# Performance work log

Measured on AMD Instinct MI355X. Metric: run time of the kernel, lower is better.

The kernel has to match this reference:

```python
import jax, jax.numpy as jnp
import numpy as np

POOL_RAD = 1.0   # init kwarg pool_rad
N = 16384        # total points
B = 8            # graphs in batch
F = 128          # feature dim
BIG = 1e30

def _voxel_keys(pos, batch, rad):
    # torch_geometric.voxel_grid with start=min-rad/2, end=max+rad/2, batch as extra dim
    start = pos.min(0) - rad * 0.5
    end = pos.max(0) + rad * 0.5
    nv = jnp.floor((end - start) / rad).astype(jnp.int32) + 1  # voxels per spatial dim
    c = jnp.floor((pos - start) / rad).astype(jnp.int32)       # [N,3] voxel coords
    lin = c[:, 0] + c[:, 1] * nv[0] + c[:, 2] * nv[0] * nv[1]
    return lin + batch.astype(jnp.int32) * (nv[0] * nv[1] * nv[2])

def _consecutive(keys, n):
    # consecutive_cluster: relabel to sorted-consecutive ids; perm = last index per cluster
    _, inv = jnp.unique(keys, return_inverse=True, size=n,
                        fill_value=jnp.iinfo(jnp.int32).max)
    inv = inv.reshape(-1)
    perm = jax.ops.segment_max(jnp.arange(n, dtype=jnp.int32), inv, num_segments=n)
    counts = jax.ops.segment_sum(jnp.ones((n,), jnp.int32), inv, num_segments=n)
    return inv, jnp.clip(perm, 0, n - 1), counts

def _nearest(pos, batch, cpos, cbatch, cvalid):
    # nearest centroid within the same graph; invalid/padded centroids masked out
    d = (pos * pos).sum(1)[:, None] - 2.0 * (pos @ cpos.T) + (cpos * cpos).sum(1)[None, :]
    ok = (batch[:, None] == cbatch[None, :]) & cvalid[None, :]
    return jnp.argmin(jnp.where(ok, d, BIG), axis=1)

def _pool(pos, x, batch):
    n = pos.shape[0]
    # stage 1: voxel-grid clustering, centroid positions
    inv1, perm1, cnt1 = _consecutive(_voxel_keys(pos, batch, POOL_RAD), n)
    c1 = jnp.maximum(cnt1, 1).astype(pos.dtype)[:, None]
    cpos = jax.ops.segment_sum(pos, inv1, num_segments=n) / c1
    cbatch = batch[perm1]
    # stage 2: reassign each point to its nearest voxel centroid, relabel
    cl2 = _nearest(jax.lax.stop_gradient(pos), batch,
                   jax.lax.stop_gradient(cpos), cbatch, cnt1 > 0)
    inv2, perm2, cnt2 = _consecutive(cl2, n)
    valid2 = cnt2 > 0
    c2 = jnp.maximum(cnt2, 1).astype(pos.dtype)[:, None]
    pos_out = jax.ops.segment_sum(pos, inv2, num_segments=n) / c2   # mean pos
    x_out = jax.ops.segment_max(x, inv2, num_segments=n)            # aggr='max'
    x_out = jnp.where(valid2[:, None], x_out, 0.0)
    pos_out = jnp.where(valid2[:, None], pos_out, 0.0)
    batch_out = jnp.where(valid2, batch[perm2], -1)
    return x_out, pos_out, batch_out

def setup_inputs():
    key = jax.random.key(0)
    k1, k2 = jax.random.split(key)
    pos = jax.random.uniform(k1, (N, 3), jnp.float32) * 10.0
    x = jax.random.normal(k2, (N, F), jnp.float32)
    batch = jnp.repeat(jnp.arange(B, dtype=jnp.int32), N // B)
    return {"pos": pos, "x": x, "batch": batch}

def reference(pos, x, batch):
    return _pool(pos, x, batch)
```

## Files before the change

### kernel.cpp

```cpp
#include <hip/hip_runtime.h>

#define TPB 256
#define K1SZ 32768
#define MAXB 256

static __device__ __forceinline__ unsigned int fmap(float f) {
  unsigned int b = __float_as_uint(f);
  return (b & 0x80000000u) ? ~b : (b | 0x80000000u);
}
static __device__ __forceinline__ float funmap(unsigned int u) {
  unsigned int b = (u & 0x80000000u) ? (u & 0x7fffffffu) : ~u;
  return __uint_as_float(b);
}

static __device__ __forceinline__ int wave_incl_scan(int v, int lane) {
  #pragma unroll
  for (int off = 1; off < 64; off <<= 1) {
    int u = __shfl_up(v, off);
    if (lane >= off) v += u;
  }
  return v;
}

__global__ void k_init(double* __restrict__ sum1, double* __restrict__ sum2,
                       int* __restrict__ cnt1, int* __restrict__ cnt2,
                       int* __restrict__ perm1, int* __restrict__ perm2,
                       int* __restrict__ flags1, int* __restrict__ flags2,
                       unsigned int* __restrict__ xacc, int n, int F) {
  int t = blockIdx.x * blockDim.x + threadIdx.x;
  if (t < n * F) xacc[t] = 0u;
  if (t < 3 * n) { sum1[t] = 0.0; sum2[t] = 0.0; }
  if (t < n) { cnt1[t] = 0; cnt2[t] = 0; perm1[t] = -1; perm2[t] = -1; flags2[t] = 0; }
  if (t < K1SZ) flags1[t] = 0;
}

__global__ __launch_bounds__(1024) void k_minmax(const float* __restrict__ pos, int n,
                                                 float* __restrict__ scal) {
  int t = threadIdx.x;
  int lane = t & 63, wid = t >> 6;
  float mn[3] = {3.4e38f, 3.4e38f, 3.4e38f};
  float mx[3] = {-3.4e38f, -3.4e38f, -3.4e38f};
  const float4* p4 = (const float4*)pos;
  int np4 = n >> 2;
  for (int j = t; j < np4; j += 1024) {
    float4 a = p4[3 * j], b = p4[3 * j + 1], c = p4[3 * j + 2];
    mn[0] = fminf(mn[0], fminf(fminf(a.x, a.w), fminf(b.z, c.y)));
    mx[0] = fmaxf(mx[0], fmaxf(fmaxf(a.x, a.w), fmaxf(b.z, c.y)));
    mn[1] = fminf(mn[1], fminf(fminf(a.y, b.x), fminf(b.w, c.z)));
    mx[1] = fmaxf(mx[1], fmaxf(fmaxf(a.y, b.x), fmaxf(b.w, c.z)));
    mn[2] = fminf(mn[2], fminf(fminf(a.z, b.y), fminf(c.x, c.w)));
    mx[2] = fmaxf(mx[2], fmaxf(fmaxf(a.z, b.y), fmaxf(c.x, c.w)));
  }
  if (t == 0) {
    for (int i = np4 * 4; i < n; ++i)
      for (int d = 0; d < 3; ++d) {
        float v = pos[i * 3 + d];
        mn[d] = fminf(mn[d], v);
        mx[d] = fmaxf(mx[d], v);
      }
  }
  #pragma unroll
  for (int off = 32; off > 0; off >>= 1) {
    #pragma unroll
    for (int d = 0; d < 3; ++d) {
      mn[d] = fminf(mn[d], __shfl_xor(mn[d], off));
      mx[d] = fmaxf(mx[d], __shfl_xor(mx[d], off));
    }
  }
  __shared__ float smn[16][3], smx[16][3];
  if (lane == 0)
    for (int d = 0; d < 3; ++d) { smn[wid][d] = mn[d]; smx[wid][d] = mx[d]; }
  __syncthreads();
  if (t == 0) {
    float rmn[3], rmx[3];
    for (int d = 0; d < 3; ++d) { rmn[d] = smn[0][d]; rmx[d] = smx[0][d]; }
    for (int w = 1; w < 16; ++w)
      for (int d = 0; d < 3; ++d) {
        rmn[d] = fminf(rmn[d], smn[w][d]);
        rmx[d] = fmaxf(rmx[d], smx[w][d]);
      }
    int* isc = (int*)(scal + 3);
    int nv[3];
    for (int d = 0; d < 3; ++d) {
      float start = rmn[d] - 0.5f;
      float end   = rmx[d] + 0.5f;
      nv[d] = (int)floorf(end - start) + 1;
      scal[d] = start;
    }
    isc[0] = nv[0];
    isc[1] = nv[0] * nv[1];
    isc[2] = nv[0] * nv[1] * nv[2];
  }
}

__global__ void k_keys(const float* __restrict__ pos, const int* __restrict__ batch, int n,
                       const float* __restrict__ scal, int* __restrict__ key1,
                       int* __restrict__ flags1) {
  int i = blockIdx.x * blockDim.x + threadIdx.x;
  if (i >= n) return;
  const int* isc = (const int*)(scal + 3);
  int c0 = (int)floorf(pos[i * 3 + 0] - scal[0]);
  int c1 = (int)floorf(pos[i * 3 + 1] - scal[1]);
  int c2 = (int)floorf(pos[i * 3 + 2] - scal[2]);
  int key = c0 + c1 * isc[0] + c2 * isc[1] + batch[i] * isc[2];
  key = min(max(key, 0), K1SZ - 1);
  key1[i] = key;
  flags1[key] = 1;
}

__global__ __launch_bounds__(1024) void k_scan(const int* __restrict__ flags,
                                               int* __restrict__ rank, int L) {
  const int t = threadIdx.x;
  const int lane = t & 63;
  const int wid = t >> 6;
  __shared__ int wsum[16];
  const int4* f4 = (const int4*)flags;
  int4* r4 = (int4*)rank;
  const int n4 = L >> 2;
  int base = 0;
  for (int tile = 0; tile * 1024 < n4; ++tile) {
    int i = tile * 1024 + t;
    int4 v = (i < n4) ? f4[i] : int4{0, 0, 0, 0};
    int p0 = v.x, p1 = p0 + v.y, p2 = p1 + v.z, p3 = p2 + v.w;
    int ws = wave_incl_scan(p3, lane);
    if (lane == 63) wsum[wid] = ws;
    __syncthreads();
    int woff = 0, ttot = 0;
    #pragma unroll
    for (int w = 0; w < 16; ++w) {
      int s = wsum[w];
      if (w < wid) woff += s;
      ttot += s;
    }
    int e = base + woff + (ws - p3);
    if (i < n4) r4[i] = int4{e, e + p0, e + p1, e + p2};
    base += ttot;
    __syncthreads();
  }
  if (t == 0) rank[L] = base;
}

__global__ void k_assign1(const float* __restrict__ pos, int n,
                          const int* __restrict__ key1, const int* __restrict__ rank1,
                          int* __restrict__ inv1, int* __restrict__ cnt1,
                          int* __restrict__ perm1, double* __restrict__ sum1) {
  int i = blockIdx.x * blockDim.x + threadIdx.x;
  if (i >= n) return;
  int c = rank1[key1[i]];
  inv1[i] = c;
  atomicAdd(&cnt1[c], 1);
  atomicMax(&perm1[c], i);
  atomicAdd(&sum1[c * 3 + 0], (double)pos[i * 3 + 0]);
  atomicAdd(&sum1[c * 3 + 1], (double)pos[i * 3 + 1]);
  atomicAdd(&sum1[c * 3 + 2], (double)pos[i * 3 + 2]);
}

__global__ void k_centroid1(int n, const int* __restrict__ cnt1,
                            double* __restrict__ sum1,
                            const int* __restrict__ rank1, const float* __restrict__ scal,
                            int* __restrict__ blo, int* __restrict__ bhi) {
  int k = blockIdx.x * blockDim.x + threadIdx.x;
  if (k < MAXB) {
    int nvtot = ((const int*)(scal + 3))[2];
    long long j0l = (long long)k * nvtot;
    long long j1l = j0l + nvtot;
    int j0 = (int)(j0l > K1SZ ? K1SZ : j0l);
    int j1 = (int)(j1l > K1SZ ? K1SZ : j1l);
    int lo = rank1[j0], hi = rank1[j1] - 1;
    blo[k] = (hi >= lo) ? lo : -1;
    bhi[k] = hi;
  }
  if (k >= n) return;
  int c = cnt1[k];
  if (c <= 0) return;
  double inv = 1.0 / (double)c;
  sum1[k * 3 + 0] *= inv;
  sum1[k * 3 + 1] *= inv;
  sum1[k * 3 + 2] *= inv;
}

__global__ void k_nearest(const float* __restrict__ pos, const int* __restrict__ batch, int n,
                          const double* __restrict__ cpos, const int* __restrict__ blo,
                          const int* __restrict__ bhi, int* __restrict__ cl2,
                          int* __restrict__ flags2) {
  int w = (blockIdx.x * blockDim.x + threadIdx.x) >> 6;
  int lane = threadIdx.x & 63;
  if (w >= n) return;
  double px = pos[w * 3 + 0], py = pos[w * 3 + 1], pz = pos[w * 3 + 2];
  int b = min(max(batch[w], 0), MAXB - 1);
  int lo = blo[b], hi = bhi[b];
  double best = 1e300;
  int bk = lo >= 0 ? lo : 0;
  if (lo >= 0) {
    for (int k = lo + lane; k <= hi; k += 64) {
      double dx = px - cpos[k * 3 + 0];
      double dy = py - cpos[k * 3 + 1];
      double dz = pz - cpos[k * 3 + 2];
      double d = dx * dx + dy * dy + dz * dz;
      if (d < best) { best = d; bk = k; }
    }
  }
  for (int off = 32; off > 0; off >>= 1) {
    double od = __shfl_down(best, off);
    int ok = __shfl_down(bk, off);
    if (od < best || (od == best && ok < bk)) { best = od; bk = ok; }
  }
  if (lane == 0) {
    cl2[w] = bk;
    flags2[bk] = 1;
  }
}

__global__ void k_assign2(const float* __restrict__ pos, int n,
                          const int* __restrict__ cl2, const int* __restrict__ rank2,
                          int* __restrict__ inv2, int* __restrict__ cnt2,
                          int* __restrict__ perm2, double* __restrict__ sum2) {
  int i = blockIdx.x * blockDim.x + threadIdx.x;
  if (i >= n) return;
  int c = rank2[cl2[i]];
  inv2[i] = c;
  atomicAdd(&cnt2[c], 1);
  atomicMax(&perm2[c], i);
  atomicAdd(&sum2[c * 3 + 0], (double)pos[i * 3 + 0]);
  atomicAdd(&sum2[c * 3 + 1], (double)pos[i * 3 + 1]);
  atomicAdd(&sum2[c * 3 + 2], (double)pos[i * 3 + 2]);
}

__global__ void k_xmax(const float* __restrict__ x, int n, int F,
                       const int* __restrict__ inv2, unsigned int* __restrict__ xacc) {
  int t = blockIdx.x * blockDim.x + threadIdx.x;
  if (t >= n * F) return;
  int i = t / F;
  int f = t - i * F;
  atomicMax(&xacc[inv2[i] * F + f], fmap(x[t]));
}

__global__ void k_finalize(int n, int F, const int* __restrict__ cnt2,
                           const int* __restrict__ perm2, const int* __restrict__ batch,
                           const double* __restrict__ sum2, unsigned int* __restrict__ xacc,
                           float* __restrict__ pos_out, float* __restrict__ batch_out) {
  int t = blockIdx.x * blockDim.x + threadIdx.x;
  if (t < n * F) {
    int j = t / F;
    float out = 0.0f;
    if (cnt2[j] > 0) out = funmap(xacc[t]);
    ((float*)xacc)[t] = out;
  }
  if (t < n) {
    int c = cnt2[t];
    if (c > 0) {
      double inv = 1.0 / (double)c;
      pos_out[t * 3 + 0] = (float)(sum2[t * 3 + 0] * inv);
      pos_out[t * 3 + 1] = (float)(sum2[t * 3 + 1] * inv);
      pos_out[t * 3 + 2] = (float)(sum2[t * 3 + 2] * inv);
      batch_out[t] = (float)batch[perm2[t]];
    } else {
      pos_out[t * 3 + 0] = 0.0f;
      pos_out[t * 3 + 1] = 0.0f;
      pos_out[t * 3 + 2] = 0.0f;
      batch_out[t] = -1.0f;
    }
  }
}

extern "C" void kernel_launch(void* const* d_in, const int* in_sizes, int n_in,
                              void* d_out, int out_size, void* d_ws, size_t ws_size,
                              hipStream_t stream) {
  const float* pos   = (const float*)d_in[0];
  const float* x     = (const float*)d_in[1];
  const int*   batch = (const int*)d_in[2];
  int n = in_sizes[2];
  int F = in_sizes[1] / n;

  char* ws = (char*)d_ws;
  size_t off = 0;
  auto alloc = [&](size_t bytes, size_t align) -> void* {
    off = (off + align - 1) & ~(align - 1);
    void* p = ws + off;
    off += bytes;
    return p;
  };
  double* sum1   = (double*)alloc((size_t)n * 3 * sizeof(double), 16);
  double* sum2   = (double*)alloc((size_t)n * 3 * sizeof(double), 16);
  int* key1      = (int*)alloc((size_t)n * 4, 16);
  int* inv1      = (int*)alloc((size_t)n * 4, 16);
  int* cnt1      = (int*)alloc((size_t)n * 4, 16);
  int* perm1     = (int*)alloc((size_t)n * 4, 16);
  int* cl2       = (int*)alloc((size_t)n * 4, 16);
  int* inv2      = (int*)alloc((size_t)n * 4, 16);
  int* cnt2      = (int*)alloc((size_t)n * 4, 16);
  int* perm2     = (int*)alloc((size_t)n * 4, 16);
  int* flags1    = (int*)alloc((size_t)K1SZ * 4, 16);
  int* rank1     = (int*)alloc(((size_t)K1SZ + 4) * 4, 16);
  int* flags2    = (int*)alloc((size_t)n * 4, 16);
  int* rank2     = (int*)alloc(((size_t)n + 4) * 4, 16);
  int* blo       = (int*)alloc((size_t)MAXB * 4, 16);
  int* bhi       = (int*)alloc((size_t)MAXB * 4, 16);
  float* scal    = (float*)alloc(64, 16);

  unsigned int* xacc = (unsigned int*)d_out;
  float* pos_out     = (float*)d_out + (size_t)n * F;
  float* batch_out   = pos_out + (size_t)n * 3;

  int nb  = (n + TPB - 1) / TPB;
  int nbF = (n * F + TPB - 1) / TPB;
  int nbW = (n * 64 + TPB - 1) / TPB;

  k_init<<<nbF, TPB, 0, stream>>>(sum1, sum2, cnt1, cnt2, perm1, perm2,
                                  flags1, flags2, xacc, n, F);
  k_minmax<<<1, 1024, 0, stream>>>(pos, n, scal);
  k_keys<<<nb, TPB, 0, stream>>>(pos, batch, n, scal, key1, flags1);
  k_scan<<<1, 1024, 0, stream>>>(flags1, rank1, K1SZ);
  k_assign1<<<nb, TPB, 0, stream>>>(pos, n, key1, rank1, inv1, cnt1, perm1, sum1);
  k_centroid1<<<nb, TPB, 0, stream>>>(n, cnt1, sum1, rank1, scal, blo, bhi);
  k_nearest<<<nbW, TPB, 0, stream>>>(pos, batch, n, sum1, blo, bhi, cl2, flags2);
  k_scan<<<1, 1024, 0, stream>>>(flags2, rank2, n);
  k_assign2<<<nb, TPB, 0, stream>>>(pos, n, cl2, rank2, inv2, cnt2, perm2, sum2);
  k_xmax<<<nbF, TPB, 0, stream>>>(x, n, F, inv2, xacc);
  k_finalize<<<nbF, TPB, 0, stream>>>(n, F, cnt2, perm2, batch, sum2, xacc,
                                      pos_out, batch_out);
}
```

Measured before the change: 78.72 us.

## Fuse minmax, key, and scan stages into one block; merge assign2 into xmax

Merges the min/max reduction, voxel-key computation, stage-1 scan and per-batch range computation into a single 1024-thread kernel, which removes several launches and global round-trips. The second assignment is folded into the feature max kernel, with the f==0 thread doing the count, perm and sum atomics. Unused inv1/perm1 arrays and their atomics are dropped. The trade-off is that key computation now runs on only one block instead of a full grid, and the xmax kernel recomputes the rank lookup for every feature element.

```diff
diff --git a/kernel.cpp b/kernel.cpp
--- a/kernel.cpp
+++ b/kernel.cpp
@@ -24,20 +24,31 @@
 
 __global__ void k_init(double* __restrict__ sum1, double* __restrict__ sum2,
                        int* __restrict__ cnt1, int* __restrict__ cnt2,
-                       int* __restrict__ perm1, int* __restrict__ perm2,
-                       int* __restrict__ flags1, int* __restrict__ flags2,
-                       unsigned int* __restrict__ xacc, int n, int F) {
+                       int* __restrict__ perm2, int* __restrict__ flags1,
+                       int* __restrict__ flags2, unsigned int* __restrict__ xacc,
+                       int n, int F) {
   int t = blockIdx.x * blockDim.x + threadIdx.x;
   if (t < n * F) xacc[t] = 0u;
   if (t < 3 * n) { sum1[t] = 0.0; sum2[t] = 0.0; }
-  if (t < n) { cnt1[t] = 0; cnt2[t] = 0; perm1[t] = -1; perm2[t] = -1; flags2[t] = 0; }
+  if (t < n) { cnt1[t] = 0; cnt2[t] = 0; perm2[t] = -1; flags2[t] = 0; }
   if (t < K1SZ) flags1[t] = 0;
 }
 
-__global__ __launch_bounds__(1024) void k_minmax(const float* __restrict__ pos, int n,
-                                                 float* __restrict__ scal) {
-  int t = threadIdx.x;
-  int lane = t & 63, wid = t >> 6;
+__global__ __launch_bounds__(1024) void k_phaseA(const float* __restrict__ pos,
+                                                 const int* __restrict__ batch, int n,
+                                                 float* __restrict__ scal,
+                                                 int* __restrict__ key1,
+                                                 int* __restrict__ flags1,
+                                                 int* __restrict__ rank1,
+                                                 int* __restrict__ blo,
+                                                 int* __restrict__ bhi) {
+  const int t = threadIdx.x;
+  const int lane = t & 63, wid = t >> 6;
+  __shared__ float smn[16][3], smx[16][3];
+  __shared__ float sstart[3];
+  __shared__ int sisc[3];
+  __shared__ int wsum[16];
+
   float mn[3] = {3.4e38f, 3.4e38f, 3.4e38f};
   float mx[3] = {-3.4e38f, -3.4e38f, -3.4e38f};
   const float4* p4 = (const float4*)pos;
@@ -67,7 +78,6 @@
       mx[d] = fmaxf(mx[d], __shfl_xor(mx[d], off));
     }
   }
-  __shared__ float smn[16][3], smx[16][3];
   if (lane == 0)
     for (int d = 0; d < 3; ++d) { smn[wid][d] = mn[d]; smx[wid][d] = mx[d]; }
   __syncthreads();
@@ -79,50 +89,44 @@
         rmn[d] = fminf(rmn[d], smn[w][d]);
         rmx[d] = fmaxf(rmx[d], smx[w][d]);
       }
-    int* isc = (int*)(scal + 3);
     int nv[3];
     for (int d = 0; d < 3; ++d) {
       float start = rmn[d] - 0.5f;
       float end   = rmx[d] + 0.5f;
       nv[d] = (int)floorf(end - start) + 1;
+      sstart[d] = start;
       scal[d] = start;
     }
-    isc[0] = nv[0];
-    isc[1] = nv[0] * nv[1];
-    isc[2] = nv[0] * nv[1] * nv[2];
-  }
-}
-
-__global__ void k_keys(const float* __restrict__ pos, const int* __restrict__ batch, int n,
-                       const float* __restrict__ scal, int* __restrict__ key1,
-                       int* __restrict__ flags1) {
-  int i = blockIdx.x * blockDim.x + threadIdx.x;
-  if (i >= n) return;
-  const int* isc = (const int*)(scal + 3);
-  int c0 = (int)floorf(pos[i * 3 + 0] - scal[0]);
-  int c1 = (int)floorf(pos[i * 3 + 1] - scal[1]);
-  int c2 = (int)floorf(pos[i * 3 + 2] - scal[2]);
-  int key = c0 + c1 * isc[0] + c2 * isc[1] + batch[i] * isc[2];
-  key = min(max(key, 0), K1SZ - 1);
-  key1[i] = key;
-  flags1[key] = 1;
-}
-
-__global__ __launch_bounds__(1024) void k_scan(const int* __restrict__ flags,
-                                               int* __restrict__ rank, int L) {
-  const int t = threadIdx.x;
-  const int lane = t & 63;
-  const int wid = t >> 6;
-  __shared__ int wsum[16];
-  const int4* f4 = (const int4*)flags;
-  int4* r4 = (int4*)rank;
-  const int n4 = L >> 2;
+    sisc[0] = nv[0];
+    sisc[1] = nv[0] * nv[1];
+    sisc[2] = nv[0] * nv[1] * nv[2];
+    int* isc = (int*)(scal + 3);
+    isc[0] = sisc[0]; isc[1] = sisc[1]; isc[2] = sisc[2];
+  }
+  __syncthreads();
+
+  const float s0 = sstart[0], s1 = sstart[1], s2 = sstart[2];
+  const int i0 = sisc[0], i1 = sisc[1], i2 = sisc[2];
+  for (int i = t; i < n; i += 1024) {
+    int c0 = (int)floorf(pos[i * 3 + 0] - s0);
+    int c1 = (int)floorf(pos[i * 3 + 1] - s1);
+    int c2 = (int)floorf(pos[i * 3 + 2] - s2);
+    int key = c0 + c1 * i0 + c2 * i1 + batch[i] * i2;
+    key = min(max(key, 0), K1SZ - 1);
+    key1[i] = key;
+    flags1[key] = 1;
+  }
+  __syncthreads();
+
+  const int4* f4 = (const int4*)flags1;
+  int4* r4 = (int4*)rank1;
+  const int n4 = K1SZ >> 2;
   int base = 0;
   for (int tile = 0; tile * 1024 < n4; ++tile) {
     int i = tile * 1024 + t;
     int4 v = (i < n4) ? f4[i] : int4{0, 0, 0, 0};
-    int p0 = v.x, p1 = p0 + v.y, p2 = p1 + v.z, p3 = p2 + v.w;
-    int ws = wave_incl_scan(p3, lane);
+    int q0 = v.x, q1 = q0 + v.y, q2 = q1 + v.z, q3 = q2 + v.w;
+    int ws = wave_incl_scan(q3, lane);
     if (lane == 63) wsum[wid] = ws;
     __syncthreads();
     int woff = 0, ttot = 0;
@@ -132,44 +136,39 @@
       if (w < wid) woff += s;
       ttot += s;
     }
-    int e = base + woff + (ws - p3);
-    if (i < n4) r4[i] = int4{e, e + p0, e + p1, e + p2};
+    int e = base + woff + (ws - q3);
+    if (i < n4) r4[i] = int4{e, e + q0, e + q1, e + q2};
     base += ttot;
     __syncthreads();
   }
-  if (t == 0) rank[L] = base;
+  if (t == 0) rank1[K1SZ] = base;
+  __syncthreads();
+
+  if (t < MAXB) {
+    long long j0l = (long long)t * i2;
+    long long j1l = j0l + i2;
+    int j0 = (int)(j0l > K1SZ ? K1SZ : j0l);
+    int j1 = (int)(j1l > K1SZ ? K1SZ : j1l);
+    int lo = rank1[j0], hi = rank1[j1] - 1;
+    blo[t] = (hi >= lo) ? lo : -1;
+    bhi[t] = hi;
+  }
 }
 
 __global__ void k_assign1(const float* __restrict__ pos, int n,
                           const int* __restrict__ key1, const int* __restrict__ rank1,
-                          int* __restrict__ inv1, int* __restrict__ cnt1,
-                          int* __restrict__ perm1, double* __restrict__ sum1) {
+                          int* __restrict__ cnt1, double* __restrict__ sum1) {
   int i = blockIdx.x * blockDim.x + threadIdx.x;
   if (i >= n) return;
   int c = rank1[key1[i]];
-  inv1[i] = c;
   atomicAdd(&cnt1[c], 1);
-  atomicMax(&perm1[c], i);
   atomicAdd(&sum1[c * 3 + 0], (double)pos[i * 3 + 0]);
   atomicAdd(&sum1[c * 3 + 1], (double)pos[i * 3 + 1]);
   atomicAdd(&sum1[c * 3 + 2], (double)pos[i * 3 + 2]);
 }
 
-__global__ void k_centroid1(int n, const int* __restrict__ cnt1,
-                            double* __restrict__ sum1,
-                            const int* __restrict__ rank1, const float* __restrict__ scal,
-                            int* __restrict__ blo, int* __restrict__ bhi) {
+__global__ void k_centroid1(int n, const int* __restrict__ cnt1, double* __restrict__ sum1) {
   int k = blockIdx.x * blockDim.x + threadIdx.x;
-  if (k < MAXB) {
-    int nvtot = ((const int*)(scal + 3))[2];
-    long long j0l = (long long)k * nvtot;
-    long long j1l = j0l + nvtot;
-    int j0 = (int)(j0l > K1SZ ? K1SZ : j0l);
-    int j1 = (int)(j1l > K1SZ ? K1SZ : j1l);
-    int lo = rank1[j0], hi = rank1[j1] - 1;
-    blo[k] = (hi >= lo) ? lo : -1;
-    bhi[k] = hi;
-  }
   if (k >= n) return;
   int c = cnt1[k];
   if (c <= 0) return;
@@ -211,28 +210,56 @@
   }
 }
 
-__global__ void k_assign2(const float* __restrict__ pos, int n,
-                          const int* __restrict__ cl2, const int* __restrict__ rank2,
-                          int* __restrict__ inv2, int* __restrict__ cnt2,
-                          int* __restrict__ perm2, double* __restrict__ sum2) {
-  int i = blockIdx.x * blockDim.x + threadIdx.x;
-  if (i >= n) return;
-  int c = rank2[cl2[i]];
-  inv2[i] = c;
-  atomicAdd(&cnt2[c], 1);
-  atomicMax(&perm2[c], i);
-  atomicAdd(&sum2[c * 3 + 0], (double)pos[i * 3 + 0]);
-  atomicAdd(&sum2[c * 3 + 1], (double)pos[i * 3 + 1]);
-  atomicAdd(&sum2[c * 3 + 2], (double)pos[i * 3 + 2]);
-}
-
-__global__ void k_xmax(const float* __restrict__ x, int n, int F,
-                       const int* __restrict__ inv2, unsigned int* __restrict__ xacc) {
+__global__ __launch_bounds__(1024) void k_scan(const int* __restrict__ flags,
+                                               int* __restrict__ rank, int L) {
+  const int t = threadIdx.x;
+  const int lane = t & 63;
+  const int wid = t >> 6;
+  __shared__ int wsum[16];
+  const int4* f4 = (const int4*)flags;
+  int4* r4 = (int4*)rank;
+  const int n4 = L >> 2;
+  int base = 0;
+  for (int tile = 0; tile * 1024 < n4; ++tile) {
+    int i = tile * 1024 + t;
+    int4 v = (i < n4) ? f4[i] : int4{0, 0, 0, 0};
+    int q0 = v.x, q1 = q0 + v.y, q2 = q1 + v.z, q3 = q2 + v.w;
+    int ws = wave_incl_scan(q3, lane);
+    if (lane == 63) wsum[wid] = ws;
+    __syncthreads();
+    int woff = 0, ttot = 0;
+    #pragma unroll
+    for (int w = 0; w < 16; ++w) {
+      int s = wsum[w];
+      if (w < wid) woff += s;
+      ttot += s;
+    }
+    int e = base + woff + (ws - q3);
+    if (i < n4) r4[i] = int4{e, e + q0, e + q1, e + q2};
+    base += ttot;
+    __syncthreads();
+  }
+  if (t == 0) rank[L] = base;
+}
+
+__global__ void k_assign2_xmax(const float* __restrict__ pos, const float* __restrict__ x,
+                               int n, int F, const int* __restrict__ cl2,
+                               const int* __restrict__ rank2, int* __restrict__ cnt2,
+                               int* __restrict__ perm2, double* __restrict__ sum2,
+                               unsigned int* __restrict__ xacc) {
   int t = blockIdx.x * blockDim.x + threadIdx.x;
   if (t >= n * F) return;
   int i = t / F;
   int f = t - i * F;
-  atomicMax(&xacc[inv2[i] * F + f], fmap(x[t]));
+  int c = rank2[cl2[i]];
+  atomicMax(&xacc[c * F + f], fmap(x[t]));
+  if (f == 0) {
+    atomicAdd(&cnt2[c], 1);
+    atomicMax(&perm2[c], i);
+    atomicAdd(&sum2[c * 3 + 0], (double)pos[i * 3 + 0]);
+    atomicAdd(&sum2[c * 3 + 1], (double)pos[i * 3 + 1]);
+    atomicAdd(&sum2[c * 3 + 2], (double)pos[i * 3 + 2]);
+  }
 }
 
 __global__ void k_finalize(int n, int F, const int* __restrict__ cnt2,
@@ -283,11 +310,8 @@
   double* sum1   = (double*)alloc((size_t)n * 3 * sizeof(double), 16);
   double* sum2   = (double*)alloc((size_t)n * 3 * sizeof(double), 16);
   int* key1      = (int*)alloc((size_t)n * 4, 16);
-  int* inv1      = (int*)alloc((size_t)n * 4, 16);
+  int* cl2       = (int*)alloc((size_t)n * 4, 16);
   int* cnt1      = (int*)alloc((size_t)n * 4, 16);
-  int* perm1     = (int*)alloc((size_t)n * 4, 16);
-  int* cl2       = (int*)alloc((size_t)n * 4, 16);
-  int* inv2      = (int*)alloc((size_t)n * 4, 16);
   int* cnt2      = (int*)alloc((size_t)n * 4, 16);
   int* perm2     = (int*)alloc((size_t)n * 4, 16);
   int* flags1    = (int*)alloc((size_t)K1SZ * 4, 16);
@@ -306,17 +330,15 @@
   int nbF = (n * F + TPB - 1) / TPB;
   int nbW = (n * 64 + TPB - 1) / TPB;
 
-  k_init<<<nbF, TPB, 0, stream>>>(sum1, sum2, cnt1, cnt2, perm1, perm2,
+  k_init<<<nbF, TPB, 0, stream>>>(sum1, sum2, cnt1, cnt2, perm2,
                                   flags1, flags2, xacc, n, F);
-  k_minmax<<<1, 1024, 0, stream>>>(pos, n, scal);
-  k_keys<<<nb, TPB, 0, stream>>>(pos, batch, n, scal, key1, flags1);
-  k_scan<<<1, 1024, 0, stream>>>(flags1, rank1, K1SZ);
-  k_assign1<<<nb, TPB, 0, stream>>>(pos, n, key1, rank1, inv1, cnt1, perm1, sum1);
-  k_centroid1<<<nb, TPB, 0, stream>>>(n, cnt1, sum1, rank1, scal, blo, bhi);
+  k_phaseA<<<1, 1024, 0, stream>>>(pos, batch, n, scal, key1, flags1, rank1, blo, bhi);
+  k_assign1<<<nb, TPB, 0, stream>>>(pos, n, key1, rank1, cnt1, sum1);
+  k_centroid1<<<nb, TPB, 0, stream>>>(n, cnt1, sum1);
   k_nearest<<<nbW, TPB, 0, stream>>>(pos, batch, n, sum1, blo, bhi, cl2, flags2);
   k_scan<<<1, 1024, 0, stream>>>(flags2, rank2, n);
-  k_assign2<<<nb, TPB, 0, stream>>>(pos, n, cl2, rank2, inv2, cnt2, perm2, sum2);
-  k_xmax<<<nbF, TPB, 0, stream>>>(x, n, F, inv2, xacc);
+  k_assign2_xmax<<<nbF, TPB, 0, stream>>>(pos, x, n, F, cl2, rank2, cnt2, perm2,
+                                          sum2, xacc);
   k_finalize<<<nbF, TPB, 0, stream>>>(n, F, cnt2, perm2, batch, sum2, xacc,
                                       pos_out, batch_out);
 }
```

Result: slower. 83.32 us (+5.8%).

## Replace brute-force nearest-centroid scan with voxel-neighborhood search and fuse kernels

Applied to the files above, without the earlier changes.

The per-point search for the nearest centroid used to scan every centroid in the graph, one wavefront per point. It now uses one thread per point that checks only the 5x5x5 neighbouring voxels, skipping voxels whose box is farther than the current best. This is exact because each voxel centroid lies inside its own voxel. The min/max reduction is folded into block 0 of the init kernel, the stage-2 assignment atomics are fused into the feature max-scatter kernel, and the unused inv1/perm1/blo/bhi buffers are dropped. The trade-off is per-thread divergence in the neighbourhood loop, and the fused kernel runs its count and position-sum atomics only on lane f==0 of each row.

```diff
diff --git a/kernel.cpp b/kernel.cpp
--- a/kernel.cpp
+++ b/kernel.cpp
@@ -2,7 +2,6 @@
 
 #define TPB 256
 #define K1SZ 32768
-#define MAXB 256
 
 static __device__ __forceinline__ unsigned int fmap(float f) {
   unsigned int b = __float_as_uint(f);
@@ -24,72 +23,74 @@
 
 __global__ void k_init(double* __restrict__ sum1, double* __restrict__ sum2,
                        int* __restrict__ cnt1, int* __restrict__ cnt2,
-                       int* __restrict__ perm1, int* __restrict__ perm2,
-                       int* __restrict__ flags1, int* __restrict__ flags2,
-                       unsigned int* __restrict__ xacc, int n, int F) {
+                       int* __restrict__ perm2, int* __restrict__ flags1,
+                       int* __restrict__ flags2, unsigned int* __restrict__ xacc,
+                       const float* __restrict__ pos, float* __restrict__ scal,
+                       int n, int F) {
   int t = blockIdx.x * blockDim.x + threadIdx.x;
   if (t < n * F) xacc[t] = 0u;
   if (t < 3 * n) { sum1[t] = 0.0; sum2[t] = 0.0; }
-  if (t < n) { cnt1[t] = 0; cnt2[t] = 0; perm1[t] = -1; perm2[t] = -1; flags2[t] = 0; }
+  if (t < n) { cnt1[t] = 0; cnt2[t] = 0; perm2[t] = -1; flags2[t] = 0; }
   if (t < K1SZ) flags1[t] = 0;
-}
-
-__global__ __launch_bounds__(1024) void k_minmax(const float* __restrict__ pos, int n,
-                                                 float* __restrict__ scal) {
-  int t = threadIdx.x;
-  int lane = t & 63, wid = t >> 6;
-  float mn[3] = {3.4e38f, 3.4e38f, 3.4e38f};
-  float mx[3] = {-3.4e38f, -3.4e38f, -3.4e38f};
-  const float4* p4 = (const float4*)pos;
-  int np4 = n >> 2;
-  for (int j = t; j < np4; j += 1024) {
-    float4 a = p4[3 * j], b = p4[3 * j + 1], c = p4[3 * j + 2];
-    mn[0] = fminf(mn[0], fminf(fminf(a.x, a.w), fminf(b.z, c.y)));
-    mx[0] = fmaxf(mx[0], fmaxf(fmaxf(a.x, a.w), fmaxf(b.z, c.y)));
-    mn[1] = fminf(mn[1], fminf(fminf(a.y, b.x), fminf(b.w, c.z)));
-    mx[1] = fmaxf(mx[1], fmaxf(fmaxf(a.y, b.x), fmaxf(b.w, c.z)));
-    mn[2] = fminf(mn[2], fminf(fminf(a.z, b.y), fminf(c.x, c.w)));
-    mx[2] = fmaxf(mx[2], fmaxf(fmaxf(a.z, b.y), fmaxf(c.x, c.w)));
-  }
-  if (t == 0) {
-    for (int i = np4 * 4; i < n; ++i)
+
+  if (blockIdx.x == 0) {
+    const int tid = threadIdx.x;
+    const int lane = tid & 63, wid = tid >> 6;
+    float mn[3] = {3.4e38f, 3.4e38f, 3.4e38f};
+    float mx[3] = {-3.4e38f, -3.4e38f, -3.4e38f};
+    const float4* p4 = (const float4*)pos;
+    int np4 = n >> 2;
+    for (int j = tid; j < np4; j += TPB) {
+      float4 a = p4[3 * j], b = p4[3 * j + 1], c = p4[3 * j + 2];
+      mn[0] = fminf(mn[0], fminf(fminf(a.x, a.w), fminf(b.z, c.y)));
+      mx[0] = fmaxf(mx[0], fmaxf(fmaxf(a.x, a.w), fmaxf(b.z, c.y)));
+      mn[1] = fminf(mn[1], fminf(fminf(a.y, b.x), fminf(b.w, c.z)));
+      mx[1] = fmaxf(mx[1], fmaxf(fmaxf(a.y, b.x), fmaxf(b.w, c.z)));
+      mn[2] = fminf(mn[2], fminf(fminf(a.z, b.y), fminf(c.x, c.w)));
+      mx[2] = fmaxf(mx[2], fmaxf(fmaxf(a.z, b.y), fmaxf(c.x, c.w)));
+    }
+    if (tid == 0) {
+      for (int i = np4 * 4; i < n; ++i)
+        for (int d = 0; d < 3; ++d) {
+          float v = pos[i * 3 + d];
+          mn[d] = fminf(mn[d], v);
+          mx[d] = fmaxf(mx[d], v);
+        }
+    }
+    #pragma unroll
+    for (int off = 32; off > 0; off >>= 1) {
+      #pragma unroll
       for (int d = 0; d < 3; ++d) {
-        float v = pos[i * 3 + d];
-        mn[d] = fminf(mn[d], v);
-        mx[d] = fmaxf(mx[d], v);
+        mn[d] = fminf(mn[d], __shfl_xor(mn[d], off));
+        mx[d] = fmaxf(mx[d], __shfl_xor(mx[d], off));
       }
-  }
-  #pragma unroll
-  for (int off = 32; off > 0; off >>= 1) {
-    #pragma unroll
-    for (int d = 0; d < 3; ++d) {
-      mn[d] = fminf(mn[d], __shfl_xor(mn[d], off));
-      mx[d] = fmaxf(mx[d], __shfl_xor(mx[d], off));
-    }
-  }
-  __shared__ float smn[16][3], smx[16][3];
-  if (lane == 0)
-    for (int d = 0; d < 3; ++d) { smn[wid][d] = mn[d]; smx[wid][d] = mx[d]; }
-  __syncthreads();
-  if (t == 0) {
-    float rmn[3], rmx[3];
-    for (int d = 0; d < 3; ++d) { rmn[d] = smn[0][d]; rmx[d] = smx[0][d]; }
-    for (int w = 1; w < 16; ++w)
+    }
+    __shared__ float smn[4][3], smx[4][3];
+    if (lane == 0)
+      for (int d = 0; d < 3; ++d) { smn[wid][d] = mn[d]; smx[wid][d] = mx[d]; }
+    __syncthreads();
+    if (tid == 0) {
+      float rmn[3], rmx[3];
+      for (int d = 0; d < 3; ++d) { rmn[d] = smn[0][d]; rmx[d] = smx[0][d]; }
+      for (int w = 1; w < 4; ++w)
+        for (int d = 0; d < 3; ++d) {
+          rmn[d] = fminf(rmn[d], smn[w][d]);
+          rmx[d] = fmaxf(rmx[d], smx[w][d]);
+        }
+      int nv[3];
       for (int d = 0; d < 3; ++d) {
-        rmn[d] = fminf(rmn[d], smn[w][d]);
-        rmx[d] = fmaxf(rmx[d], smx[w][d]);
+        float start = rmn[d] - 0.5f;
+        float end   = rmx[d] + 0.5f;
+        nv[d] = (int)floorf(end - start) + 1;
+        scal[d] = start;
       }
-    int* isc = (int*)(scal + 3);
-    int nv[3];
-    for (int d = 0; d < 3; ++d) {
-      float start = rmn[d] - 0.5f;
-      float end   = rmx[d] + 0.5f;
-      nv[d] = (int)floorf(end - start) + 1;
-      scal[d] = start;
-    }
-    isc[0] = nv[0];
-    isc[1] = nv[0] * nv[1];
-    isc[2] = nv[0] * nv[1] * nv[2];
+      int* isc = (int*)(scal + 3);
+      isc[0] = nv[0];
+      isc[1] = nv[0] * nv[1];
+      isc[2] = nv[0] * nv[1] * nv[2];
+      isc[3] = nv[1];
+      isc[4] = nv[2];
+    }
   }
 }
 
@@ -121,8 +122,8 @@
   for (int tile = 0; tile * 1024 < n4; ++tile) {
     int i = tile * 1024 + t;
     int4 v = (i < n4) ? f4[i] : int4{0, 0, 0, 0};
-    int p0 = v.x, p1 = p0 + v.y, p2 = p1 + v.z, p3 = p2 + v.w;
-    int ws = wave_incl_scan(p3, lane);
+    int q0 = v.x, q1 = q0 + v.y, q2 = q1 + v.z, q3 = q2 + v.w;
+    int ws = wave_incl_scan(q3, lane);
     if (lane == 63) wsum[wid] = ws;
     __syncthreads();
     int woff = 0, ttot = 0;
@@ -132,44 +133,27 @@
       if (w < wid) woff += s;
       ttot += s;
     }
-    int e = base + woff + (ws - p3);
-    if (i < n4) r4[i] = int4{e, e + p0, e + p1, e + p2};
+    int e = base + woff + (ws - q3);
+    if (i < n4) r4[i] = int4{e, e + q0, e + q1, e + q2};
     base += ttot;
     __syncthreads();
   }
-  if (t == 0) rank[L] = base;
 }
 
 __global__ void k_assign1(const float* __restrict__ pos, int n,
                           const int* __restrict__ key1, const int* __restrict__ rank1,
-                          int* __restrict__ inv1, int* __restrict__ cnt1,
-                          int* __restrict__ perm1, double* __restrict__ sum1) {
+                          int* __restrict__ cnt1, double* __restrict__ sum1) {
   int i = blockIdx.x * blockDim.x + threadIdx.x;
   if (i >= n) return;
   int c = rank1[key1[i]];
-  inv1[i] = c;
   atomicAdd(&cnt1[c], 1);
-  atomicMax(&perm1[c], i);
   atomicAdd(&sum1[c * 3 + 0], (double)pos[i * 3 + 0]);
   atomicAdd(&sum1[c * 3 + 1], (double)pos[i * 3 + 1]);
   atomicAdd(&sum1[c * 3 + 2], (double)pos[i * 3 + 2]);
 }
 
-__global__ void k_centroid1(int n, const int* __restrict__ cnt1,
-                            double* __restrict__ sum1,
-                            const int* __restrict__ rank1, const float* __restrict__ scal,
-                            int* __restrict__ blo, int* __restrict__ bhi) {
+__global__ void k_centroid1(int n, const int* __restrict__ cnt1, double* __restrict__ sum1) {
   int k = blockIdx.x * blockDim.x + threadIdx.x;
-  if (k < MAXB) {
-    int nvtot = ((const int*)(scal + 3))[2];
-    long long j0l = (long long)k * nvtot;
-    long long j1l = j0l + nvtot;
-    int j0 = (int)(j0l > K1SZ ? K1SZ : j0l);
-    int j1 = (int)(j1l > K1SZ ? K1SZ : j1l);
-    int lo = rank1[j0], hi = rank1[j1] - 1;
-    blo[k] = (hi >= lo) ? lo : -1;
-    bhi[k] = hi;
-  }
   if (k >= n) return;
   int c = cnt1[k];
   if (c <= 0) return;
@@ -180,59 +164,82 @@
 }
 
 __global__ void k_nearest(const float* __restrict__ pos, const int* __restrict__ batch, int n,
-                          const double* __restrict__ cpos, const int* __restrict__ blo,
-                          const int* __restrict__ bhi, int* __restrict__ cl2,
-                          int* __restrict__ flags2) {
-  int w = (blockIdx.x * blockDim.x + threadIdx.x) >> 6;
-  int lane = threadIdx.x & 63;
-  if (w >= n) return;
-  double px = pos[w * 3 + 0], py = pos[w * 3 + 1], pz = pos[w * 3 + 2];
-  int b = min(max(batch[w], 0), MAXB - 1);
-  int lo = blo[b], hi = bhi[b];
-  double best = 1e300;
-  int bk = lo >= 0 ? lo : 0;
-  if (lo >= 0) {
-    for (int k = lo + lane; k <= hi; k += 64) {
-      double dx = px - cpos[k * 3 + 0];
-      double dy = py - cpos[k * 3 + 1];
-      double dz = pz - cpos[k * 3 + 2];
-      double d = dx * dx + dy * dy + dz * dz;
-      if (d < best) { best = d; bk = k; }
-    }
-  }
-  for (int off = 32; off > 0; off >>= 1) {
-    double od = __shfl_down(best, off);
-    int ok = __shfl_down(bk, off);
-    if (od < best || (od == best && ok < bk)) { best = od; bk = ok; }
-  }
-  if (lane == 0) {
-    cl2[w] = bk;
-    flags2[bk] = 1;
-  }
-}
-
-__global__ void k_assign2(const float* __restrict__ pos, int n,
-                          const int* __restrict__ cl2, const int* __restrict__ rank2,
-                          int* __restrict__ inv2, int* __restrict__ cnt2,
-                          int* __restrict__ perm2, double* __restrict__ sum2) {
+                          const double* __restrict__ cpos, const int* __restrict__ flags1,
+                          const int* __restrict__ rank1, const float* __restrict__ scal,
+                          int* __restrict__ cl2, int* __restrict__ flags2) {
   int i = blockIdx.x * blockDim.x + threadIdx.x;
   if (i >= n) return;
-  int c = rank2[cl2[i]];
-  inv2[i] = c;
-  atomicAdd(&cnt2[c], 1);
-  atomicMax(&perm2[c], i);
-  atomicAdd(&sum2[c * 3 + 0], (double)pos[i * 3 + 0]);
-  atomicAdd(&sum2[c * 3 + 1], (double)pos[i * 3 + 1]);
-  atomicAdd(&sum2[c * 3 + 2], (double)pos[i * 3 + 2]);
-}
-
-__global__ void k_xmax(const float* __restrict__ x, int n, int F,
-                       const int* __restrict__ inv2, unsigned int* __restrict__ xacc) {
+  const int* isc = (const int*)(scal + 3);
+  const float s0 = scal[0], s1 = scal[1], s2 = scal[2];
+  const int nv0 = isc[0], nv01 = isc[1], nvtot = isc[2];
+  const int nv1 = isc[3], nv2 = isc[4];
+  float pxf = pos[i * 3 + 0], pyf = pos[i * 3 + 1], pzf = pos[i * 3 + 2];
+  double px = pxf, py = pyf, pz = pzf;
+  int c0 = (int)floorf(pxf - s0);
+  int c1 = (int)floorf(pyf - s1);
+  int c2 = (int)floorf(pzf - s2);
+  int base = batch[i] * nvtot;
+  int k0 = min(max(c0 + c1 * nv0 + c2 * nv01 + base, 0), K1SZ - 1);
+  int bid = rank1[k0];
+  double dx = px - cpos[bid * 3 + 0];
+  double dy = py - cpos[bid * 3 + 1];
+  double dz = pz - cpos[bid * 3 + 2];
+  double best2 = dx * dx + dy * dy + dz * dz;
+  for (int oz = -2; oz <= 2; ++oz) {
+    int z = c2 + oz;
+    if (z < 0 || z >= nv2) continue;
+    double lz = (double)s2 + z;
+    double gz = fmax(0.0, fmax(lz - pz, pz - (lz + 1.0)));
+    double gz2 = gz * gz;
+    if (gz2 > best2 + 1e-4) continue;
+    for (int oy = -2; oy <= 2; ++oy) {
+      int y = c1 + oy;
+      if (y < 0 || y >= nv1) continue;
+      double ly = (double)s1 + y;
+      double gy = fmax(0.0, fmax(ly - py, py - (ly + 1.0)));
+      double gzy2 = gz2 + gy * gy;
+      if (gzy2 > best2 + 1e-4) continue;
+      for (int ox = -2; ox <= 2; ++ox) {
+        int xq = c0 + ox;
+        if (xq < 0 || xq >= nv0) continue;
+        if ((ox | oy | oz) == 0) continue;
+        double lx = (double)s0 + xq;
+        double gx = fmax(0.0, fmax(lx - px, px - (lx + 1.0)));
+        double mind2 = gzy2 + gx * gx;
+        if (mind2 > best2 + 1e-4) continue;
+        int key = min(xq + y * nv0 + z * nv01 + base, K1SZ - 1);
+        if (!flags1[key]) continue;
+        int c = rank1[key];
+        double ddx = px - cpos[c * 3 + 0];
+        double ddy = py - cpos[c * 3 + 1];
+        double ddz = pz - cpos[c * 3 + 2];
+        double d2 = ddx * ddx + ddy * ddy + ddz * ddz;
+        if (d2 < best2 || (d2 == best2 && c < bid)) { best2 = d2; bid = c; }
+      }
+    }
+  }
+  cl2[i] = bid;
+  flags2[bid] = 1;
+}
+
+__global__ void k_assign2_xmax(const float* __restrict__ pos, const float* __restrict__ x,
+                               int n, int F, const int* __restrict__ cl2,
+                               const int* __restrict__ rank2, int* __restrict__ cnt2,
+                               int* __restrict__ perm2, double* __restrict__ sum2,
+                               unsigned int* __restrict__ xacc) {
   int t = blockIdx.x * blockDim.x + threadIdx.x;
   if (t >= n * F) return;
   int i = t / F;
   int f = t - i * F;
-  atomicMax(&xacc[inv2[i] * F + f], fmap(x[t]));
+  int c = rank2[cl2[i]];
+  atomicMax(&xacc[c * F + f], fmap(x[t]));
+  if (f == 0) {
+    atomicAdd(&cnt2[c], 1);
+    atomicMax(&perm2[c], i);
+    atomicAdd(&sum2[c * 3 + 0], (double)pos[i * 3 + 0]);
+    atomicAdd(&sum2[c * 3 + 1], (double)pos[i * 3 + 1]);
+    atomicAdd(&sum2[c * 3 + 2], (double)pos[i * 3 + 2]);
+  }
 }
 
 __global__ void k_finalize(int n, int F, const int* __restrict__ cnt2,
@@ -283,19 +290,14 @@
   double* sum1   = (double*)alloc((size_t)n * 3 * sizeof(double), 16);
   double* sum2   = (double*)alloc((size_t)n * 3 * sizeof(double), 16);
   int* key1      = (int*)alloc((size_t)n * 4, 16);
-  int* inv1      = (int*)alloc((size_t)n * 4, 16);
+  int* cl2       = (int*)alloc((size_t)n * 4, 16);
   int* cnt1      = (int*)alloc((size_t)n * 4, 16);
-  int* perm1     = (int*)alloc((size_t)n * 4, 16);
-  int* cl2       = (int*)alloc((size_t)n * 4, 16);
-  int* inv2      = (int*)alloc((size_t)n * 4, 16);
   int* cnt2      = (int*)alloc((size_t)n * 4, 16);
   int* perm2     = (int*)alloc((size_t)n * 4, 16);
   int* flags1    = (int*)alloc((size_t)K1SZ * 4, 16);
-  int* rank1     = (int*)alloc(((size_t)K1SZ + 4) * 4, 16);
+  int* rank1     = (int*)alloc((size_t)K1SZ * 4, 16);
   int* flags2    = (int*)alloc((size_t)n * 4, 16);
-  int* rank2     = (int*)alloc(((size_t)n + 4) * 4, 16);
-  int* blo       = (int*)alloc((size_t)MAXB * 4, 16);
-  int* bhi       = (int*)alloc((size_t)MAXB * 4, 16);
+  int* rank2     = (int*)alloc((size_t)n * 4, 16);
   float* scal    = (float*)alloc(64, 16);
 
   unsigned int* xacc = (unsigned int*)d_out;
@@ -304,19 +306,18 @@
 
   int nb  = (n + TPB - 1) / TPB;
   int nbF = (n * F + TPB - 1) / TPB;
-  int nbW = (n * 64 + TPB - 1) / TPB;
-
-  k_init<<<nbF, TPB, 0, stream>>>(sum1, sum2, cnt1, cnt2, perm1, perm2,
-                                  flags1, flags2, xacc, n, F);
-  k_minmax<<<1, 1024, 0, stream>>>(pos, n, scal);
+  int nbP = (n + 63) / 64;
+
+  k_init<<<nbF, TPB, 0, stream>>>(sum1, sum2, cnt1, cnt2, perm2,
+                                  flags1, flags2, xacc, pos, scal, n, F);
   k_keys<<<nb, TPB, 0, stream>>>(pos, batch, n, scal, key1, flags1);
   k_scan<<<1, 1024, 0, stream>>>(flags1, rank1, K1SZ);
-  k_assign1<<<nb, TPB, 0, stream>>>(pos, n, key1, rank1, inv1, cnt1, perm1, sum1);
-  k_centroid1<<<nb, TPB, 0, stream>>>(n, cnt1, sum1, rank1, scal, blo, bhi);
-  k_nearest<<<nbW, TPB, 0, stream>>>(pos, batch, n, sum1, blo, bhi, cl2, flags2);
+  k_assign1<<<nb, TPB, 0, stream>>>(pos, n, key1, rank1, cnt1, sum1);
+  k_centroid1<<<nb, TPB, 0, stream>>>(n, cnt1, sum1);
+  k_nearest<<<nbP, 64, 0, stream>>>(pos, batch, n, sum1, flags1, rank1, scal, cl2, flags2);
   k_scan<<<1, 1024, 0, stream>>>(flags2, rank2, n);
-  k_assign2<<<nb, TPB, 0, stream>>>(pos, n, cl2, rank2, inv2, cnt2, perm2, sum2);
-  k_xmax<<<nbF, TPB, 0, stream>>>(x, n, F, inv2, xacc);
+  k_assign2_xmax<<<nbF, TPB, 0, stream>>>(pos, x, n, F, cl2, rank2, cnt2, perm2,
+                                          sum2, xacc);
   k_finalize<<<nbF, TPB, 0, stream>>>(n, F, cnt2, perm2, batch, sum2, xacc,
                                       pos_out, batch_out);
 }
```

New measurement: 67.15 us. 14.7% less time.
